# Optimization experiments

Measured on AMD Instinct MI355X. Metric: run time of the kernel, lower is better.

The kernel has to match this reference:

```python
import jax, jax.numpy as jnp
import numpy as np

N_NODES = 100000
N_EDGES = 640000
IN_CH, HID_CH, OUT_CH = 256, 128, 64


def setup_inputs() -> dict:
    key = jax.random.key(0)
    ks = jax.random.split(key, 6)
    x = jax.random.normal(ks[0], (N_NODES, IN_CH), dtype=jnp.float32)
    edge_index = jax.random.randint(ks[1], (2, N_EDGES), 0, N_NODES, dtype=jnp.int32)
    # Glorot-style init for GCNConv weights
    W1 = jax.random.normal(ks[2], (IN_CH, HID_CH), dtype=jnp.float32) * (1.0 / np.sqrt(IN_CH))
    W_mu = jax.random.normal(ks[3], (HID_CH, OUT_CH), dtype=jnp.float32) * (1.0 / np.sqrt(HID_CH))
    W_logvar = jax.random.normal(ks[4], (HID_CH, OUT_CH), dtype=jnp.float32) * (1.0 / np.sqrt(HID_CH))
    return {
        "x": x,
        "edge_index": edge_index,
        "W1": W1,
        "b1": jnp.zeros((HID_CH,), jnp.float32),
        "W_mu": W_mu,
        "b_mu": jnp.zeros((OUT_CH,), jnp.float32),
        "W_logvar": W_logvar,
        "b_logvar": jnp.zeros((OUT_CH,), jnp.float32),
    }


def reference(x, edge_index, W1, b1, W_mu, b_mu, W_logvar, b_logvar):
    N = x.shape[0]
    # PyG GCNConv default: add self-loops, symmetric normalization D^-1/2 A_hat D^-1/2
    loops = jnp.arange(N, dtype=edge_index.dtype)
    src = jnp.concatenate([edge_index[0], loops])  # [E+N]
    dst = jnp.concatenate([edge_index[1], loops])  # [E+N]
    deg = jax.ops.segment_sum(jnp.ones_like(src, dtype=x.dtype), dst, num_segments=N)
    dinv = jax.lax.rsqrt(deg)  # deg >= 1 due to self-loops
    norm = dinv[src] * dinv[dst]  # [E+N]

    def gcn_conv(h, W, b):
        h = h @ W                                   # [N, d_out]
        msg = h[src] * norm[:, None]                # gather + scale  [E+N, d_out]
        out = jax.ops.segment_sum(msg, dst, num_segments=N)  # scatter-add
        return out + b

    h = jax.nn.relu(gcn_conv(x, W1, b1))
    mu = gcn_conv(h, W_mu, b_mu)
    logvar = gcn_conv(h, W_logvar, b_logvar)
    return (mu, logvar)
```

## Files before the change

kernel.cpp:

```cpp
#include <hip/hip_runtime.h>
#include <hip/hip_bf16.h>

#define N_NODES 100000
#define E_EDGES 640000

typedef __attribute__((ext_vector_type(8))) short short8;
typedef __attribute__((ext_vector_type(4))) float float4v;

__device__ __forceinline__ float bf2f(unsigned int u16) {
    union { unsigned int i; float f; } c; c.i = u16 << 16; return c.f;
}
__device__ __forceinline__ unsigned short f2bf(float f) {
    union { float f; unsigned int i; } c; c.f = f;
    unsigned int x = c.i;
    unsigned int r = (x + 0x7fffu + ((x >> 16) & 1u)) >> 16;
    return (unsigned short)r;
}

#define ASYNC16NT(g, l)                                                        \
    __builtin_amdgcn_global_load_lds(                                          \
        (const __attribute__((address_space(1))) void*)(g),                    \
        (__attribute__((address_space(3))) void*)(l), 16, 0, 2)

#define WS_HIST    0
#define WS_CURSOR  524288
#define WS_OFFS    1048576
#define WS_DINV    1572864
#define WS_BSUMS   2097152
#define WS_EIDX    2621440
#define WS_WP1     7864320
#define WS_WP2     7929856
#define WS_H0      7962624
#define WS_H       33562624

#define NB_E 2500
__global__ __launch_bounds__(256) void k_hist_pack(const int* __restrict__ dst, int* __restrict__ hist,
                                                   const float* __restrict__ W1,
                                                   const float* __restrict__ Wmu,
                                                   const float* __restrict__ Wlv,
                                                   unsigned short* __restrict__ Wp1,
                                                   unsigned short* __restrict__ Wp2) {
    int b = blockIdx.x;
    if (b < NB_E) {
        int e = b * 256 + threadIdx.x;
        if (e < E_EDGES) atomicAdd(&hist[__builtin_nontemporal_load(dst + e)], 1);
    } else {
        int i = (b - NB_E) * 256 + threadIdx.x;
        if (i < 256 * 128) {
            int k = i >> 7, n = i & 127;
            Wp1[n * 256 + k] = f2bf(W1[i]);
        }
        if (i < 128 * 128) {
            int k = i >> 7, n = i & 127;
            float w = (n < 64) ? Wmu[k * 64 + n] : Wlv[k * 64 + (n - 64)];
            Wp2[n * 128 + k] = f2bf(w);
        }
    }
}

__global__ __launch_bounds__(256) void k_scan1(const int* __restrict__ hist,
                                               int* __restrict__ offs,
                                               int* __restrict__ bsums,
                                               float* __restrict__ dinv) {
    __shared__ int sd[256];
    int t = threadIdx.x;
    int base = blockIdx.x * 1024 + t * 4;
    int v[4];
#pragma unroll
    for (int j = 0; j < 4; ++j) v[j] = (base + j < N_NODES) ? hist[base + j] : 0;
#pragma unroll
    for (int j = 0; j < 4; ++j)
        if (base + j < N_NODES) dinv[base + j] = rsqrtf((float)(v[j] + 1));
    int s = v[0] + v[1] + v[2] + v[3];
    sd[t] = s;
    __syncthreads();
    for (int d = 1; d < 256; d <<= 1) {
        int x = (t >= d) ? sd[t - d] : 0;
        __syncthreads();
        sd[t] += x;
        __syncthreads();
    }
    int excl = sd[t] - s;
    if (t == 255) bsums[blockIdx.x] = sd[255];
    int run = excl;
#pragma unroll
    for (int j = 0; j < 4; ++j) {
        if (base + j < N_NODES) offs[base + j] = run;
        run += v[j];
    }
}

__global__ __launch_bounds__(128) void k_scan2(int* __restrict__ bsums, int nb) {
    __shared__ int sd[128];
    int t = threadIdx.x;
    int v = (t < nb) ? bsums[t] : 0;
    sd[t] = v;
    __syncthreads();
    for (int d = 1; d < 128; d <<= 1) {
        int x = (t >= d) ? sd[t - d] : 0;
        __syncthreads();
        sd[t] += x;
        __syncthreads();
    }
    if (t < nb) bsums[t] = sd[t] - v;
}

__global__ __launch_bounds__(256) void k_fill(const int* __restrict__ src, const int* __restrict__ dst,
                                              const int* __restrict__ offs, const int* __restrict__ bsums,
                                              int* __restrict__ cursor,
                                              const float* __restrict__ dinv,
                                              int2* __restrict__ eidx) {
    int e = blockIdx.x * 256 + threadIdx.x;
    if (e < E_EDGES) {
        int s = __builtin_nontemporal_load(src + e);
        int d = __builtin_nontemporal_load(dst + e);
        int p = offs[d] + bsums[d >> 10] + atomicAdd(&cursor[d], 1);
        int2 v;
        v.x = s;
        v.y = __float_as_int(dinv[s] * dinv[d]);
        eidx[p] = v;
    }
}

__global__ __launch_bounds__(256, 6) void k_mgemm1(const float* __restrict__ A,
                                                   const unsigned short* __restrict__ Bpack,
                                                   unsigned short* __restrict__ out) {
    __shared__ float As[64 * 32];
    __shared__ unsigned short Bs[128 * 40];
    int tid = threadIdx.x;
    int row0 = blockIdx.x * 64;
    int wave = tid >> 6, lane = tid & 63;
    int c = lane & 15, q = lane >> 4;
    int wrow = (wave >> 1) * 32, wcol = (wave & 1) * 64;

    float4v acc[2][4];
#pragma unroll
    for (int i = 0; i < 2; ++i)
#pragma unroll
        for (int j = 0; j < 4; ++j) acc[i][j] = (float4v){0.f, 0.f, 0.f, 0.f};

    int srow = tid >> 1;
    int shalf = (tid & 1) * 16;

    for (int k0 = 0; k0 < 256; k0 += 32) {
        const unsigned short* bsrc = Bpack + (size_t)srow * 256 + k0 + shalf;
        short8 b0 = *(const short8*)(bsrc);
        short8 b1 = *(const short8*)(bsrc + 8);
#pragma unroll
        for (int t = 0; t < 2; ++t) {
            int grp = t * 4 + wave;
            int S = grp * 64 + lane;
            int row = S >> 3, j = S & 7;
            int kq = j ^ (row & 7);
            const float* g = A + (size_t)(row0 + row) * 256 + k0 + kq * 4;
            float* ldst = As + grp * 256;
            if (row0 + row < N_NODES) ASYNC16NT(g, ldst);
        }
        *(short8*)(&Bs[srow * 40 + shalf])     = b0;
        *(short8*)(&Bs[srow * 40 + shalf + 8]) = b1;
        __syncthreads();

        short8 af[2], bfr[4];
#pragma unroll
        for (int mt = 0; mt < 2; ++mt) {
            int r = wrow + mt * 16 + c;
            int j0 = (q * 2) ^ (r & 7);
            float4v fa = *(const float4v*)(&As[r * 32 + j0 * 4]);
            float4v fb = *(const float4v*)(&As[r * 32 + (j0 ^ 1) * 4]);
            short8 s;
#pragma unroll
            for (int jj = 0; jj < 4; ++jj) s[jj]     = (short)f2bf(fa[jj]);
#pragma unroll
            for (int jj = 0; jj < 4; ++jj) s[4 + jj] = (short)f2bf(fb[jj]);
            af[mt] = s;
        }
#pragma unroll
        for (int nt = 0; nt < 4; ++nt)
            bfr[nt] = *(const short8*)(&Bs[(wcol + nt * 16 + c) * 40 + q * 8]);
#pragma unroll
        for (int mt = 0; mt < 2; ++mt)
#pragma unroll
            for (int nt = 0; nt < 4; ++nt)
                acc[mt][nt] = __builtin_amdgcn_mfma_f32_16x16x32_bf16(af[mt], bfr[nt], acc[mt][nt], 0, 0, 0);
        __syncthreads();
    }

#pragma unroll
    for (int mt = 0; mt < 2; ++mt) {
#pragma unroll
        for (int i = 0; i < 4; ++i) {
            int row = row0 + wrow + mt * 16 + q * 4 + i;
            if (row >= N_NODES) continue;
#pragma unroll
            for (int nt = 0; nt < 4; ++nt) {
                int cc = wcol + nt * 16 + c;
                out[(size_t)row * 128 + cc] = f2bf(acc[mt][nt][i]);
            }
        }
    }
}

__global__ __launch_bounds__(256) void k_agg1(const unsigned int* __restrict__ in,
                                              unsigned int* __restrict__ out,
                                              const float* __restrict__ dinv,
                                              const int2* __restrict__ eidx,
                                              const int* __restrict__ offs,
                                              const int* __restrict__ bsums,
                                              const int* __restrict__ cnt,
                                              const float* __restrict__ bias) {
    int wid = (blockIdx.x * 256 + threadIdx.x) >> 6;
    if (wid >= N_NODES) return;
    int l = threadIdx.x & 63;
    float di = dinv[wid];
    unsigned int u = in[(size_t)wid * 64 + l];
    float sc = di * di;
    float ax = sc * bf2f(u & 0xffffu) + bias[2 * l];
    float ay = sc * bf2f(u >> 16) + bias[2 * l + 1];
    int start = offs[wid] + bsums[wid >> 10];
    int n = cnt[wid];

    for (int base = 0; base < n; base += 64) {
        int m = min(n - base, 64);
        int sreg = 0; float wreg = 0.f;
        if (l < m) {
            int2 ev = eidx[start + base + l];
            sreg = ev.x;
            wreg = __int_as_float(ev.y);
        }
        int e = 0;
        for (; e + 4 <= m; e += 4) {
            int s0 = __shfl(sreg, e),     s1 = __shfl(sreg, e + 1);
            int s2 = __shfl(sreg, e + 2), s3 = __shfl(sreg, e + 3);
            float w0 = __shfl(wreg, e),     w1 = __shfl(wreg, e + 1);
            float w2 = __shfl(wreg, e + 2), w3 = __shfl(wreg, e + 3);
            unsigned int u0 = in[(size_t)s0 * 64 + l];
            unsigned int u1 = in[(size_t)s1 * 64 + l];
            unsigned int u2 = in[(size_t)s2 * 64 + l];
            unsigned int u3 = in[(size_t)s3 * 64 + l];
            ax += w0 * bf2f(u0 & 0xffffu); ay += w0 * bf2f(u0 >> 16);
            ax += w1 * bf2f(u1 & 0xffffu); ay += w1 * bf2f(u1 >> 16);
            ax += w2 * bf2f(u2 & 0xffffu); ay += w2 * bf2f(u2 >> 16);
            ax += w3 * bf2f(u3 & 0xffffu); ay += w3 * bf2f(u3 >> 16);
        }
        for (; e < m; ++e) {
            int s0 = __shfl(sreg, e);
            float w0 = __shfl(wreg, e);
            unsigned int u0 = in[(size_t)s0 * 64 + l];
            ax += w0 * bf2f(u0 & 0xffffu); ay += w0 * bf2f(u0 >> 16);
        }
    }
    ax = fmaxf(ax, 0.f); ay = fmaxf(ay, 0.f);
    out[(size_t)wid * 64 + l] = (unsigned int)f2bf(ax) | ((unsigned int)f2bf(ay) << 16);
}

__global__ __launch_bounds__(512, 8) void k_agg2mm(const unsigned int* __restrict__ in,
                                                   const float* __restrict__ dinv,
                                                   const int2* __restrict__ eidx,
                                                   const int* __restrict__ offs,
                                                   const int* __restrict__ bsums,
                                                   const int* __restrict__ cnt,
                                                   const unsigned short* __restrict__ Bpack,
                                                   const float* __restrict__ bias0,
                                                   const float* __restrict__ bias1,
                                                   float* __restrict__ out) {
    __shared__ unsigned short As4[4 * 64 * 40];
    __shared__ unsigned short Bs[128 * 40];
    int tid = threadIdx.x;
    int row0 = blockIdx.x * 64;
    int wave = tid >> 6, lane = tid & 63;
    int l = lane;

    unsigned int* As4w = (unsigned int*)As4;
    int ui = (l >> 4) * 1280 + (l & 15);
#pragma unroll 1
    for (int i = 0; i < 8; ++i) {
        int lr = wave * 8 + i;
        int nd = row0 + lr;
        float ax = 0.f, ay = 0.f;
        if (nd < N_NODES) {
            float di = dinv[nd];
            unsigned int u = in[(size_t)nd * 64 + l];
            float sc = di * di;
            ax = sc * bf2f(u & 0xffffu);
            ay = sc * bf2f(u >> 16);
            int start = offs[nd] + bsums[nd >> 10];
            int n = cnt[nd];
            for (int base = 0; base < n; base += 64) {
                int m = min(n - base, 64);
                int sreg = 0; float wreg = 0.f;
                if (l < m) {
                    int2 ev = eidx[start + base + l];
                    sreg = ev.x;
                    wreg = __int_as_float(ev.y);
                }
                int e = 0;
                for (; e + 4 <= m; e += 4) {
                    int s0 = __shfl(sreg, e),     s1 = __shfl(sreg, e + 1);
                    int s2 = __shfl(sreg, e + 2), s3 = __shfl(sreg, e + 3);
                    float w0 = __shfl(wreg, e),     w1 = __shfl(wreg, e + 1);
                    float w2 = __shfl(wreg, e + 2), w3 = __shfl(wreg, e + 3);
                    unsigned int u0 = in[(size_t)s0 * 64 + l];
                    unsigned int u1 = in[(size_t)s1 * 64 + l];
                    unsigned int u2 = in[(size_t)s2 * 64 + l];
                    unsigned int u3 = in[(size_t)s3 * 64 + l];
                    ax += w0 * bf2f(u0 & 0xffffu); ay += w0 * bf2f(u0 >> 16);
                    ax += w1 * bf2f(u1 & 0xffffu); ay += w1 * bf2f(u1 >> 16);
                    ax += w2 * bf2f(u2 & 0xffffu); ay += w2 * bf2f(u2 >> 16);
                    ax += w3 * bf2f(u3 & 0xffffu); ay += w3 * bf2f(u3 >> 16);
                }
                for (; e < m; ++e) {
                    int s0 = __shfl(sreg, e);
                    float w0 = __shfl(wreg, e);
                    unsigned int u0 = in[(size_t)s0 * 64 + l];
                    ax += w0 * bf2f(u0 & 0xffffu); ay += w0 * bf2f(u0 >> 16);
                }
            }
        }
        As4w[ui + lr * 20] = (unsigned int)f2bf(ax) | ((unsigned int)f2bf(ay) << 16);
    }

    int c = lane & 15, q = lane >> 4;
    int wm = wave >> 2, wn = wave & 3;
    int wrow = wm * 32, wcol = wn * 32;

    float4v acc[2][2];
#pragma unroll
    for (int i = 0; i < 2; ++i)
#pragma unroll
        for (int j = 0; j < 2; ++j) acc[i][j] = (float4v){0.f, 0.f, 0.f, 0.f};

    int srow = tid >> 2;
    int soff = (tid & 3) * 8;

    for (int kc = 0; kc < 4; ++kc) {
        int k0 = kc * 32;
        short8 b0 = *(const short8*)(Bpack + (size_t)srow * 128 + k0 + soff);
        __syncthreads();
        *(short8*)(&Bs[srow * 40 + soff]) = b0;
        __syncthreads();

        short8 af[2], bfr[2];
#pragma unroll
        for (int mt = 0; mt < 2; ++mt)
            af[mt] = *(const short8*)(&As4[kc * 2560 + (wrow + mt * 16 + c) * 40 + q * 8]);
#pragma unroll
        for (int nt = 0; nt < 2; ++nt)
            bfr[nt] = *(const short8*)(&Bs[(wcol + nt * 16 + c) * 40 + q * 8]);
#pragma unroll
        for (int mt = 0; mt < 2; ++mt)
#pragma unroll
            for (int nt = 0; nt < 2; ++nt)
                acc[mt][nt] = __builtin_amdgcn_mfma_f32_16x16x32_bf16(af[mt], bfr[nt], acc[mt][nt], 0, 0, 0);
    }

#pragma unroll
    for (int mt = 0; mt < 2; ++mt) {
#pragma unroll
        for (int i = 0; i < 4; ++i) {
            int row = row0 + wrow + mt * 16 + q * 4 + i;
            if (row >= N_NODES) continue;
#pragma unroll
            for (int nt = 0; nt < 2; ++nt) {
                int cc = wcol + nt * 16 + c;
                float v = acc[mt][nt][i];
                if (cc < 64) out[(size_t)row * 64 + cc] = v + bias0[cc];
                else out[(size_t)N_NODES * 64 + (size_t)row * 64 + (cc - 64)] = v + bias1[cc - 64];
            }
        }
    }
}

extern "C" void kernel_launch(void* const* d_in, const int* in_sizes, int n_in,
                              void* d_out, int out_size, void* d_ws, size_t ws_size,
                              hipStream_t stream) {
    const float* x    = (const float*)d_in[0];
    const int*   ei   = (const int*)d_in[1];
    const float* W1   = (const float*)d_in[2];
    const float* b1   = (const float*)d_in[3];
    const float* Wmu  = (const float*)d_in[4];
    const float* bmu  = (const float*)d_in[5];
    const float* Wlv  = (const float*)d_in[6];
    const float* blv  = (const float*)d_in[7];
    float* outp = (float*)d_out;

    const int* src = ei;
    const int* dst = ei + E_EDGES;

    char* ws = (char*)d_ws;
    int*            hist   = (int*)(ws + WS_HIST);
    int*            cursor = (int*)(ws + WS_CURSOR);
    int*            offs   = (int*)(ws + WS_OFFS);
    float*          dinv   = (float*)(ws + WS_DINV);
    int*            bsums  = (int*)(ws + WS_BSUMS);
    int2*           eidx   = (int2*)(ws + WS_EIDX);
    unsigned short* Wp1    = (unsigned short*)(ws + WS_WP1);
    unsigned short* Wp2    = (unsigned short*)(ws + WS_WP2);
    unsigned short* h0     = (unsigned short*)(ws + WS_H0);
    unsigned short* h      = (unsigned short*)(ws + WS_H);

    const int NB_S = (N_NODES + 1023) / 1024;
    const int NB_G = (N_NODES + 63) / 64;

    hipMemsetAsync(ws + WS_HIST, 0, 1048576, stream);
    k_hist_pack<<<NB_E + 128, 256, 0, stream>>>(dst, hist, W1, Wmu, Wlv, Wp1, Wp2);
    k_scan1<<<NB_S, 256, 0, stream>>>(hist, offs, bsums, dinv);
    k_scan2<<<1, 128, 0, stream>>>(bsums, NB_S);
    k_fill<<<NB_E, 256, 0, stream>>>(src, dst, offs, bsums, cursor, dinv, eidx);

    k_mgemm1<<<NB_G, 256, 0, stream>>>(x, Wp1, h0);
    k_agg1<<<(N_NODES * 64 + 255) / 256, 256, 0, stream>>>(
        (const unsigned int*)h0, (unsigned int*)h, dinv, eidx, offs, bsums, hist, b1);

    k_agg2mm<<<NB_G, 512, 0, stream>>>(
        (const unsigned int*)h, dinv, eidx, offs, bsums, hist, Wp2, bmu, blv, outp);
}
```

Measured before the change: 339.1 us.

## Fuse block-sum scan into scan1 and edge fill into first GEMM

```diff
diff --git a/kernel.cpp b/kernel.cpp
--- a/kernel.cpp
+++ b/kernel.cpp
@@ -24,6 +24,7 @@
 
 #define WS_HIST    0
 #define WS_CURSOR  524288
+#define WS_DONE    1048512
 #define WS_OFFS    1048576
 #define WS_DINV    1572864
 #define WS_BSUMS   2097152
@@ -34,6 +35,7 @@
 #define WS_H       33562624
 
 #define NB_E 2500
+#define NB_G 1563
 __global__ __launch_bounds__(256) void k_hist_pack(const int* __restrict__ dst, int* __restrict__ hist,
                                                    const float* __restrict__ W1,
                                                    const float* __restrict__ Wmu,
@@ -61,8 +63,10 @@
 __global__ __launch_bounds__(256) void k_scan1(const int* __restrict__ hist,
                                                int* __restrict__ offs,
                                                int* __restrict__ bsums,
-                                               float* __restrict__ dinv) {
+                                               float* __restrict__ dinv,
+                                               int* __restrict__ done) {
     __shared__ int sd[256];
+    __shared__ int isLast;
     int t = threadIdx.x;
     int base = blockIdx.x * 1024 + t * 4;
     int v[4];
@@ -81,52 +85,56 @@
         __syncthreads();
     }
     int excl = sd[t] - s;
-    if (t == 255) bsums[blockIdx.x] = sd[255];
+    if (t == 255) atomicExch(&bsums[blockIdx.x], sd[255]);
     int run = excl;
 #pragma unroll
     for (int j = 0; j < 4; ++j) {
         if (base + j < N_NODES) offs[base + j] = run;
         run += v[j];
     }
-}
-
-__global__ __launch_bounds__(128) void k_scan2(int* __restrict__ bsums, int nb) {
-    __shared__ int sd[128];
-    int t = threadIdx.x;
-    int v = (t < nb) ? bsums[t] : 0;
-    sd[t] = v;
     __syncthreads();
-    for (int d = 1; d < 128; d <<= 1) {
-        int x = (t >= d) ? sd[t - d] : 0;
-        __syncthreads();
-        sd[t] += x;
-        __syncthreads();
-    }
-    if (t < nb) bsums[t] = sd[t] - v;
-}
-
-__global__ __launch_bounds__(256) void k_fill(const int* __restrict__ src, const int* __restrict__ dst,
-                                              const int* __restrict__ offs, const int* __restrict__ bsums,
-                                              int* __restrict__ cursor,
-                                              const float* __restrict__ dinv,
-                                              int2* __restrict__ eidx) {
-    int e = blockIdx.x * 256 + threadIdx.x;
-    if (e < E_EDGES) {
-        int s = __builtin_nontemporal_load(src + e);
-        int d = __builtin_nontemporal_load(dst + e);
-        int p = offs[d] + bsums[d >> 10] + atomicAdd(&cursor[d], 1);
-        int2 v;
-        v.x = s;
-        v.y = __float_as_int(dinv[s] * dinv[d]);
-        eidx[p] = v;
-    }
-}
-
-__global__ __launch_bounds__(256, 6) void k_mgemm1(const float* __restrict__ A,
-                                                   const unsigned short* __restrict__ Bpack,
-                                                   unsigned short* __restrict__ out) {
+    if (t == 0) isLast = (atomicAdd(done, 1) == (int)gridDim.x - 1);
+    __syncthreads();
+    if (isLast) {
+        int nb = gridDim.x;
+        int bv = (t < nb) ? atomicAdd(&bsums[t], 0) : 0;
+        sd[t] = bv;
+        __syncthreads();
+        for (int d = 1; d < 256; d <<= 1) {
+            int x = (t >= d) ? sd[t - d] : 0;
+            __syncthreads();
+            sd[t] += x;
+            __syncthreads();
+        }
+        if (t < nb) atomicExch(&bsums[t], sd[t] - bv);
+    }
+}
+
+__global__ __launch_bounds__(256, 6) void k_mm1_fill(const float* __restrict__ A,
+                                                     const unsigned short* __restrict__ Bpack,
+                                                     unsigned short* __restrict__ out,
+                                                     const int* __restrict__ src, const int* __restrict__ dst,
+                                                     const int* __restrict__ offs, const int* __restrict__ bsums,
+                                                     int* __restrict__ cursor,
+                                                     const float* __restrict__ dinv,
+                                                     int2* __restrict__ eidx) {
     __shared__ float As[64 * 32];
     __shared__ unsigned short Bs[128 * 40];
+
+    if (blockIdx.x >= NB_G) {
+        int e = (blockIdx.x - NB_G) * 256 + threadIdx.x;
+        if (e < E_EDGES) {
+            int s = __builtin_nontemporal_load(src + e);
+            int d = __builtin_nontemporal_load(dst + e);
+            int p = offs[d] + bsums[d >> 10] + atomicAdd(&cursor[d], 1);
+            int2 v;
+            v.x = s;
+            v.y = __float_as_int(dinv[s] * dinv[d]);
+            eidx[p] = v;
+        }
+        return;
+    }
+
     int tid = threadIdx.x;
     int row0 = blockIdx.x * 64;
     int wave = tid >> 6, lane = tid & 63;
@@ -389,6 +397,7 @@
     char* ws = (char*)d_ws;
     int*            hist   = (int*)(ws + WS_HIST);
     int*            cursor = (int*)(ws + WS_CURSOR);
+    int*            done   = (int*)(ws + WS_DONE);
     int*            offs   = (int*)(ws + WS_OFFS);
     float*          dinv   = (float*)(ws + WS_DINV);
     int*            bsums  = (int*)(ws + WS_BSUMS);
@@ -399,15 +408,14 @@
     unsigned short* h      = (unsigned short*)(ws + WS_H);
 
     const int NB_S = (N_NODES + 1023) / 1024;
-    const int NB_G = (N_NODES + 63) / 64;
 
     hipMemsetAsync(ws + WS_HIST, 0, 1048576, stream);
     k_hist_pack<<<NB_E + 128, 256, 0, stream>>>(dst, hist, W1, Wmu, Wlv, Wp1, Wp2);
-    k_scan1<<<NB_S, 256, 0, stream>>>(hist, offs, bsums, dinv);
-    k_scan2<<<1, 128, 0, stream>>>(bsums, NB_S);
-    k_fill<<<NB_E, 256, 0, stream>>>(src, dst, offs, bsums, cursor, dinv, eidx);
-
-    k_mgemm1<<<NB_G, 256, 0, stream>>>(x, Wp1, h0);
+    k_scan1<<<NB_S, 256, 0, stream>>>(hist, offs, bsums, dinv, done);
+
+    k_mm1_fill<<<NB_G + NB_E, 256, 0, stream>>>(x, Wp1, h0,
+                                                src, dst, offs, bsums, cursor, dinv, eidx);
+
     k_agg1<<<(N_NODES * 64 + 255) / 256, 256, 0, stream>>>(
         (const unsigned int*)h0, (unsigned int*)h, dinv, eidx, offs, bsums, hist, b1);
 
```

New measurement: 336.7 us. Within noise of the previous version (-0.7%).
